# Performance work log

Hardware: AMD Instinct MI355X
Metric: run time of the kernel (lower is better)

Reference implementation:

```python
import jax, jax.numpy as jnp
import numpy as np

B, NO, NM, NV, E = 16, 512, 128, 64, 256
H, DK, MS, FF = 16, 16, 8, 512
TRANS_MAX = 100.0


def _ln(x):
    m = x.mean(-1, keepdims=True)
    v = ((x - m) ** 2).mean(-1, keepdims=True)
    return (x - m) * jax.lax.rsqrt(v + 1e-5)


def _inv_norm(x):
    # 1 - minmax-normalize over the whole per-batch matrix
    mn = x.min(axis=(1, 2), keepdims=True)
    mx = x.max(axis=(1, 2), keepdims=True)
    return 1.0 - (x - mn) / (mx - mn)


def _adjacency(proc_time, trans_time, MVpair_trans, mask_dyn, mask_ma):
    # masked copy of proc_time
    A_proc = jnp.where(mask_dyn, proc_time, 0.0)
    # keep only the per-row minimum nonzero entry (min_ProcTime_elements)
    nz = jnp.where(A_proc == 0.0, jnp.inf, A_proc)
    mn = nz.min(axis=2, keepdims=True)
    keep = (A_proc == mn) & (A_proc != 0.0)
    A_proc = A_proc * keep.astype(proc_time.dtype)
    A_proc_norm = (A_proc > 0.0).astype(proc_time.dtype)
    # machine-machine masks
    mask2 = mask_ma[:, None, :] & mask_ma[:, :, None]  # [B, nm, nm]
    A_procing = (~mask2).astype(proc_time.dtype)
    A_off = _inv_norm(MVpair_trans)
    tt = jnp.where(mask2, trans_time, TRANS_MAX + 1.0)
    A_on = _inv_norm(tt)
    return A_proc_norm, A_procing, A_off, A_on


def _block(row, col, cost, Wq, Wk, Wv, Wo, mW1, mb1, mW2, mb2, fW1, fb1, fW2, fb2):
    # MatNet-style mixed-score multi-head attention encoding block
    Bb, R, _ = row.shape
    C = col.shape[1]
    q = (row @ Wq).reshape(Bb, R, H, DK).transpose(0, 2, 1, 3)  # bhrd
    k = (col @ Wk).reshape(Bb, C, H, DK).transpose(0, 2, 1, 3)  # bhcd
    v = (col @ Wv).reshape(Bb, C, H, DK).transpose(0, 2, 1, 3)
    dot = jnp.einsum('bhrd,bhcd->bhrc', q, k) / jnp.sqrt(jnp.asarray(DK, row.dtype))
    two = jnp.stack([dot, jnp.broadcast_to(cost[:, None], dot.shape)], axis=-1)  # [B,H,R,C,2]
    hmix = jax.nn.relu(jnp.einsum('bhrct,hts->bhrcs', two, mW1) + mb1[None, :, None, None, :])
    score = jnp.einsum('bhrcs,hso->bhrco', hmix, mW2)[..., 0] + mb2[:, 0][None, :, None, None]
    attn = jax.nn.softmax(score, axis=-1)
    ctx = jnp.einsum('bhrc,bhcd->bhrd', attn, v).transpose(0, 2, 1, 3).reshape(Bb, R, H * DK)
    out1 = _ln(row + ctx @ Wo)
    ffn = jax.nn.relu(out1 @ fW1 + fb1) @ fW2 + fb2
    return _ln(out1 + ffn)


def setup_inputs() -> dict:
    key = jax.random.key(0)
    ks = jax.random.split(key, 24)

    def nrm(i, shape, s=0.05):
        return jax.random.normal(ks[i], shape, jnp.float32) * s

    return {
        'ope_emb': nrm(0, (B, NO, E), 1.0),
        'ma_emb': nrm(1, (B, NM, E), 1.0),
        'veh_emb': nrm(2, (B, NV, E), 1.0),
        'proc_time': jax.random.uniform(ks[3], (B, NO, NM), jnp.float32) * 20.0,
        'offload_trans_time': jax.random.uniform(ks[4], (B, NO, NV), jnp.float32) * TRANS_MAX,
        'trans_time': jax.random.uniform(ks[5], (B, NM, NM), jnp.float32) * TRANS_MAX,
        'MVpair_trans': jax.random.uniform(ks[6], (B, NV, NM), jnp.float32) * TRANS_MAX,
        'mask_dyn_ope_ma_adj': jax.random.bernoulli(ks[7], 0.3, (B, NO, NM)),
        'mask_ma': jax.random.bernoulli(ks[8], 0.7, (B, NM)),
        # stacked params for the 4 blocks: 0=ope, 1=veh, 2=ma1, 3=ma2
        'Wq': nrm(9, (4, E, H * DK)),
        'Wk': nrm(10, (4, E, H * DK)),
        'Wv': nrm(11, (4, E, H * DK)),
        'Wo': nrm(12, (4, H * DK, E)),
        'mixW1': nrm(13, (4, H, 2, MS), 0.3),
        'mixb1': jnp.zeros((4, H, MS), jnp.float32),
        'mixW2': nrm(14, (4, H, MS, 1), 0.3),
        'mixb2': jnp.zeros((4, H, 1), jnp.float32),
        'ffW1': nrm(15, (4, E, FF)),
        'ffb1': jnp.zeros((4, FF), jnp.float32),
        'ffW2': nrm(16, (4, FF, E)),
        'ffb2': jnp.zeros((4, E), jnp.float32),
        'maprojW': nrm(17, (2 * E, E)),
        'maprojb': jnp.zeros((E,), jnp.float32),
    }


def reference(ope_emb, ma_emb, veh_emb, proc_time, offload_trans_time, trans_time,
              MVpair_trans, mask_dyn_ope_ma_adj, mask_ma,
              Wq, Wk, Wv, Wo, mixW1, mixb1, mixW2, mixb2,
              ffW1, ffb1, ffW2, ffb2, maprojW, maprojb):
    A_proc_norm, A_procing, A_off, A_on = _adjacency(
        proc_time, trans_time, MVpair_trans, mask_dyn_ope_ma_adj, mask_ma)

    def blk(i, row, col, cost):
        return _block(row, col, cost, Wq[i], Wk[i], Wv[i], Wo[i],
                      mixW1[i], mixb1[i], mixW2[i], mixb2[i],
                      ffW1[i], ffb1[i], ffW2[i], ffb2[i])

    ope_out = blk(0, ope_emb, ma_emb, A_proc_norm)
    veh_out = blk(1, veh_emb, ma_emb, A_off)
    ma1 = blk(2, ma_emb, ma_emb, A_procing)
    ma2 = blk(3, ma_emb, ma_emb, A_on)
    ma_out = jnp.concatenate([ma1, ma2], axis=-1) @ maprojW + maprojb
    return (ope_out, ma_out, veh_out)
```

## Files before the change

kernel.cpp:

```cpp
#include <hip/hip_runtime.h>
#include <hip/hip_fp16.h>
#include <hip/hip_bf16.h>


typedef unsigned short u16;
typedef __attribute__((ext_vector_type(8))) short bf16x8;
typedef __attribute__((ext_vector_type(4))) float f32x4;
struct us4 { u16 x, y, z, w; };

__device__ __forceinline__ float bf2f(u16 u) {
  return __uint_as_float(((unsigned int)u) << 16);
}
__device__ __forceinline__ u16 f2bf(float f) {
  unsigned int x = __float_as_uint(f);
  x += 0x7FFFu + ((x >> 16) & 1u);
  return (u16)(x >> 16);
}
__device__ __forceinline__ __half2 h2max(__half2 a, __half2 b) {
  unsigned au = *(unsigned*)&a, bu = *(unsigned*)&b, ru;
  asm("v_pk_max_f16 %0, %1, %2" : "=v"(ru) : "v"(au), "v"(bu));
  return *(__half2*)&ru;
}

#define NBATCH 16
#define NOPE   512
#define NMA    128
#define NVEH   64
#define EDIM   256

struct PrepArgs {
  const float* ope; const float* ma; const float* veh;
  u16* ope_bf; u16* ma_bf; u16* veh_bf;
  const float* proc; const int* mask_dyn; float* A_proc;
  const float* mv; const float* trans; const int* mask_ma;
  unsigned int* mm;
};
struct TrArgs {
  const float* Wq; const float* Wk; const float* Wv; const float* Wo;
  const float* ffW1; const float* ffW2; const float* maproj;
  u16* WqT; u16* WkT; u16* WvT; u16* WoT; u16* ffW1T; u16* ffW2T; u16* maprojT;
};
__global__ __launch_bounds__(256) void prep_a(PrepArgs a, TrArgs tr) {
  int blk = blockIdx.x, t = threadIdx.x;
  if (blk < 2816) {
    int i = blk * 256 + t;
    const float* s; u16* d; int j;
    if (i < 524288)      { s = a.ope; d = a.ope_bf; j = i; }
    else if (i < 655360) { s = a.ma;  d = a.ma_bf;  j = i - 524288; }
    else                 { s = a.veh; d = a.veh_bf; j = i - 655360; }
    float4 v = ((const float4*)s)[j];
    us4 o = { f2bf(v.x), f2bf(v.y), f2bf(v.z), f2bf(v.w) };
    ((us4*)d)[j] = o;
    return;
  }
  if (blk < 6912) {
    int local = blk - 2816;
    int row = local * 2 + (t >> 7);
    int lane = t & 127;
    size_t idx = (size_t)row * NMA + lane;
    float av = a.mask_dyn[idx] ? a.proc[idx] : 0.0f;
    float cand = (av != 0.0f) ? av : 1.0e30f;
    __shared__ float red[256];
    red[t] = cand;
    __syncthreads();
    for (int s = 64; s > 0; s >>= 1) {
      if (lane < s) red[t] = fminf(red[t], red[t + s]);
      __syncthreads();
    }
    float mn = red[t & 128];
    a.A_proc[idx] = (av != 0.0f && av == mn) ? 1.0f : 0.0f;
    return;
  }
  if (blk < 7104) {
    __shared__ float smn[256], smx[256];
    float mn = 1.0e30f, mx = -1.0e30f;
    int mmIdx;
    if (blk < 6976) {
      int local = blk - 6912;
      int b = local >> 2, chunk = local & 3;
      const float* xb = a.mv + (size_t)b * 8192 + chunk * 2048;
#pragma unroll
      for (int r = 0; r < 8; r++) {
        float v = xb[r * 256 + t];
        mn = fminf(mn, v);
        mx = fmaxf(mx, v);
      }
      mmIdx = b;
    } else {
      int local = blk - 6976;
      int b = local >> 3, chunk = local & 7;
      __shared__ unsigned char mrow[NMA];
      if (t < NMA) mrow[t] = (unsigned char)(a.mask_ma[(size_t)b * NMA + t] != 0);
      __syncthreads();
      const float* tb = a.trans + (size_t)b * 16384 + chunk * 2048;
      int rbase = chunk * 16;
#pragma unroll
      for (int r = 0; r < 8; r++) {
        int off = r * 256 + t;
        int row = rbase + (off >> 7), col = off & 127;
        bool m2 = mrow[row] && mrow[col];
        float tt = m2 ? tb[off] : 101.0f;
        mn = fminf(mn, tt);
        mx = fmaxf(mx, tt);
      }
      mmIdx = 16 + b;
    }
    smn[t] = mn; smx[t] = mx;
    __syncthreads();
    for (int s = 128; s > 0; s >>= 1) {
      if (t < s) {
        smn[t] = fminf(smn[t], smn[t + s]);
        smx[t] = fmaxf(smx[t], smx[t + s]);
      }
      __syncthreads();
    }
    if (t == 0) {
      atomicMin(&a.mm[mmIdx], __float_as_uint(smn[0]));
      atomicMax(&a.mm[32 + mmIdx], __float_as_uint(smx[0]));
    }
    return;
  }
  {
    int b2 = blk - 7104;
    const float* src; u16* dst; int Kd, Nd, tile;
    if (b2 < 1024) {
      int w = b2 >> 8, i = (b2 >> 6) & 3; tile = b2 & 63;
      const float* sw = (w == 0 ? tr.Wq : w == 1 ? tr.Wk : w == 2 ? tr.Wv : tr.Wo);
      u16* dw = (w == 0 ? tr.WqT : w == 1 ? tr.WkT : w == 2 ? tr.WvT : tr.WoT);
      src = sw + (size_t)i * 65536; dst = dw + (size_t)i * 65536;
      Kd = 256; Nd = 256;
    } else if (b2 < 1536) {
      int z = (b2 - 1024) >> 7; tile = (b2 - 1024) & 127;
      src = tr.ffW1 + (size_t)z * 131072; dst = tr.ffW1T + (size_t)z * 131072;
      Kd = 256; Nd = 512;
    } else {
      int z = (b2 - 1536) >> 7; tile = (b2 - 1536) & 127;
      if (z < 4) { src = tr.ffW2 + (size_t)z * 131072; dst = tr.ffW2T + (size_t)z * 131072; }
      else       { src = tr.maproj; dst = tr.maprojT; }
      Kd = 512; Nd = 256;
    }
    int nx = Nd >> 5;
    int k0 = (tile / nx) * 32, n0 = (tile % nx) * 32;
    __shared__ float tl[32][33];
    int tx = t & 31, ty = t >> 5;
#pragma unroll
    for (int r = 0; r < 4; r++)
      tl[ty + r * 8][tx] = src[(size_t)(k0 + ty + r * 8) * Nd + n0 + tx];
    __syncthreads();
#pragma unroll
    for (int r = 0; r < 4; r++)
      dst[(size_t)(n0 + ty + r * 8) * Kd + k0 + tx] = f2bf(tl[tx][ty + r * 8]);
  }
}

struct PB {
  const float* mv; const float* trans; const int* mask_ma;
  const unsigned int* mm; float* A_offb; float* a_on; float* a_pcing;
};
__device__ __forceinline__ void prep_b_body(const PB& p, int blk, int t) {
  if (blk < 512) {
    int b = blk >> 5, off = (blk & 31) * 256 + t;
    float lo = __uint_as_float(p.mm[b]);
    float inv = 1.0f / (__uint_as_float(p.mm[32 + b]) - lo);
    size_t idx = (size_t)b * 8192 + off;
    p.A_offb[idx] = 1.0f - (p.mv[idx] - lo) * inv;
    return;
  }
  int local = blk - 512;
  int b = local >> 6, off = (local & 63) * 256 + t;
  int row = off >> 7, col = off & 127;
  bool m2 = (p.mask_ma[(size_t)b * NMA + row] != 0) &&
            (p.mask_ma[(size_t)b * NMA + col] != 0);
  size_t idx = (size_t)b * 16384 + off;
  float tt = m2 ? p.trans[idx] : 101.0f;
  float lo = __uint_as_float(p.mm[16 + b]);
  float inv = 1.0f / (__uint_as_float(p.mm[48 + b]) - lo);
  p.a_on[idx] = 1.0f - (tt - lo) * inv;
  p.a_pcing[idx] = m2 ? 0.0f : 1.0f;
}

struct GG {
  const u16* A; const u16* WT; const float* bias; u16* C;
  int M, N, K, epi, wgStart, cshift, mode;
};
struct GGArgs { GG g[12]; PB pb; int n; int nGemmWG; };

__global__ __launch_bounds__(256) void gemm_grouped(GGArgs args) {
  int wg = blockIdx.x;
  if (wg >= args.nGemmWG) {
    prep_b_body(args.pb, wg - args.nGemmWG, threadIdx.x);
    return;
  }
  int gi = 0;
  for (int i = 1; i < args.n; i++)
    if (wg >= args.g[i].wgStart) gi = i;
  GG gg = args.g[gi];
  int lwg = wg - gg.wgStart;
  int bx = lwg & ((1 << gg.cshift) - 1);
  int by = lwg >> gg.cshift;
  int N = gg.N, K = gg.K;

  __shared__ u16 As[128][40];
  __shared__ u16 Bs[128][40];
  int tid = threadIdx.x;
  int lane = tid & 63, wid = tid >> 6;
  int wr = (wid >> 1) * 64, wc = (wid & 1) * 64;
  int m16 = lane & 15, quad = lane >> 4;
  int rb = by * 128, cb = bx * 128;
  int srow = tid >> 2;
  int schunk = (tid & 3) * 8;

  f32x4 acc[4][4];
#pragma unroll
  for (int i = 0; i < 4; i++)
#pragma unroll
    for (int j = 0; j < 4; j++) acc[i][j] = (f32x4){0.f, 0.f, 0.f, 0.f};

  for (int k0 = 0; k0 < K; k0 += 32) {
    uint4 va0 = *(const uint4*)(gg.A + (size_t)(rb + srow) * K + k0 + schunk);
    uint4 va1 = *(const uint4*)(gg.A + (size_t)(rb + 64 + srow) * K + k0 + schunk);
    uint4 vb0 = *(const uint4*)(gg.WT + (size_t)(cb + srow) * K + k0 + schunk);
    uint4 vb1 = *(const uint4*)(gg.WT + (size_t)(cb + 64 + srow) * K + k0 + schunk);
    __syncthreads();
    *(uint4*)&As[srow][schunk] = va0;
    *(uint4*)&As[64 + srow][schunk] = va1;
    *(uint4*)&Bs[srow][schunk] = vb0;
    *(uint4*)&Bs[64 + srow][schunk] = vb1;
    __syncthreads();
    bf16x8 af[4], bfr[4];
#pragma unroll
    for (int i = 0; i < 4; i++)
      af[i] = *(const bf16x8*)&As[wr + i * 16 + m16][quad * 8];
#pragma unroll
    for (int j = 0; j < 4; j++)
      bfr[j] = *(const bf16x8*)&Bs[wc + j * 16 + m16][quad * 8];
#pragma unroll
    for (int i = 0; i < 4; i++)
#pragma unroll
      for (int j = 0; j < 4; j++)
        acc[i][j] = __builtin_amdgcn_mfma_f32_16x16x32_bf16(
            af[i], bfr[j], acc[i][j], 0, 0, 0);
  }

#pragma unroll
  for (int i = 0; i < 4; i++) {
#pragma unroll
    for (int j = 0; j < 4; j++) {
      int col = cb + wc + j * 16 + m16;
      float bv = (gg.epi >= 1) ? gg.bias[col] : 0.0f;
      if (gg.mode == 3) {
        int row0 = rb + wr + i * 16 + quad * 4;
        int b = row0 >> 7, c0 = row0 & 127;
        us4 o = { f2bf(acc[i][j][0]), f2bf(acc[i][j][1]),
                  f2bf(acc[i][j][2]), f2bf(acc[i][j][3]) };
        *(us4*)(gg.C + (size_t)b * 32768 + (size_t)col * 128 + c0) = o;
      } else {
#pragma unroll
        for (int r = 0; r < 4; r++) {
          int row = rb + wr + i * 16 + quad * 4 + r;
          float v = acc[i][j][r] + bv;
          if (gg.epi == 2) v = fmaxf(v, 0.0f);
          size_t off;
          if (gg.mode == 0) {
            off = (size_t)row * N + col;
          } else if (gg.mode == 1) {
            off = ((size_t)(row >> 4)) * 4096 + (size_t)(col >> 4) * 256 +
                  (size_t)(row & 15) * 16 + (col & 15);
          } else {
            off = ((size_t)(row >> 7)) * 32768 + (size_t)(col >> 4) * 2048 +
                  (size_t)(row & 127) * 16 + (col & 15);
          }
          gg.C[off] = f2bf(v);
        }
      }
    }
  }
}

__global__ __launch_bounds__(256) void gemm_mfma_f32(
    const u16* __restrict__ A, const u16* __restrict__ WT,
    const float* __restrict__ bias, float* __restrict__ C,
    int M, int N, int K) {
  __shared__ u16 As[64][40];
  __shared__ u16 Bs[64][40];
  int tid = threadIdx.x;
  int lane = tid & 63, wid = tid >> 6;
  int wr = (wid >> 1) * 32, wc = (wid & 1) * 32;
  int m16 = lane & 15, quad = lane >> 4;
  int rb = blockIdx.y * 64, cb = blockIdx.x * 64;
  int srow = tid >> 2;
  int schunk = (tid & 3) * 8;
  f32x4 acc[2][2];
#pragma unroll
  for (int i = 0; i < 2; i++)
#pragma unroll
    for (int j = 0; j < 2; j++) acc[i][j] = (f32x4){0.f, 0.f, 0.f, 0.f};
  for (int k0 = 0; k0 < K; k0 += 32) {
    uint4 va = *(const uint4*)(A + (size_t)(rb + srow) * K + k0 + schunk);
    uint4 vb = *(const uint4*)(WT + (size_t)(cb + srow) * K + k0 + schunk);
    __syncthreads();
    *(uint4*)&As[srow][schunk] = va;
    *(uint4*)&Bs[srow][schunk] = vb;
    __syncthreads();
    bf16x8 af[2], bfr[2];
#pragma unroll
    for (int i = 0; i < 2; i++)
      af[i] = *(const bf16x8*)&As[wr + i * 16 + m16][quad * 8];
#pragma unroll
    for (int j = 0; j < 2; j++)
      bfr[j] = *(const bf16x8*)&Bs[wc + j * 16 + m16][quad * 8];
#pragma unroll
    for (int i = 0; i < 2; i++)
#pragma unroll
      for (int j = 0; j < 2; j++)
        acc[i][j] = __builtin_amdgcn_mfma_f32_16x16x32_bf16(
            af[i], bfr[j], acc[i][j], 0, 0, 0);
  }
#pragma unroll
  for (int i = 0; i < 2; i++)
#pragma unroll
    for (int j = 0; j < 2; j++) {
      int col = cb + wc + j * 16 + m16;
      float bv = bias[col];
#pragma unroll
      for (int r = 0; r < 4; r++) {
        int row = rb + wr + i * 16 + quad * 4 + r;
        C[(size_t)row * N + col] = acc[i][j][r] + bv;
      }
    }
}

struct AG {
  const u16* q; const u16* k; const u16* vT; const float* cost; u16* ctx;
  const float* w1; const float* b1; const float* w2; const float* b2;
  int R, wgStart;
};
struct AGArgs { AG g[4]; };

#define CSTRIDE 134

__global__ __launch_bounds__(256) void attn_grouped(AGArgs args) {
  int blk = blockIdx.x;
  int gi = 0;
#pragma unroll
  for (int i = 1; i < 4; i++)
    if (blk >= args.g[i].wgStart) gi = i;
  AG gg = args.g[gi];
  int local = blk - gg.wgStart;

  int t = threadIdx.x;
  int wave = t >> 6, lane = t & 63;
  int quad = lane >> 4, l16 = lane & 15;
  int j = local & 15;
  int b = (j & 7) * 2 + (j >> 3);
  int hgrp = (local >> 4) & 1;
  int tile = local >> 5;
  int m0 = b * gg.R + tile * 16;

  __shared__ __half costs_h[16 * CSTRIDE];
  __shared__ u16 pbuf[4][16 * 136];

  const float* cp = gg.cost + (size_t)m0 * 128;
  for (int i = t; i < 2048; i += 256)
    costs_h[(i >> 7) * CSTRIDE + (i & 127)] = __float2half(cp[i]);
  __syncthreads();

  const bf16x8 zerof = (bf16x8){0, 0, 0, 0, 0, 0, 0, 0};
  const f32x4 zacc = (f32x4){0.f, 0.f, 0.f, 0.f};
  const __half2 zh = __float2half2_rn(0.0f);
  u16* pb = pbuf[wave];
  const u16* qtile = gg.q + ((size_t)(m0 >> 4)) * 4096;
  const u16* kb    = gg.k + (size_t)b * 32768;

#pragma unroll
  for (int hh = 0; hh < 2; hh++) {
    int h = hgrp * 8 + wave * 2 + hh;

    __half2 w10h[8], w11h[8], b1h[8], w2h[8];
#pragma unroll
    for (int s = 0; s < 8; s++) {
      w10h[s] = __float2half2_rn(gg.w1[h * 16 + s] * 0.25f);
      w11h[s] = __float2half2_rn(gg.w1[h * 16 + 8 + s]);
      b1h[s]  = __float2half2_rn(gg.b1[h * 8 + s]);
      w2h[s]  = __float2half2_rn(gg.w2[h * 8 + s]);
    }
    float wb2v = gg.b2[h];

    bf16x8 bq = zerof;
    if (quad < 2)
      bq = *(const bf16x8*)(qtile + (size_t)h * 256 + l16 * 16 + quad * 8);
    f32x4 st[8];
    __builtin_amdgcn_s_setprio(1);
#pragma unroll
    for (int ct = 0; ct < 8; ct++) {
      bf16x8 ak = zerof;
      if (quad < 2)
        ak = *(const bf16x8*)(kb + (size_t)h * 2048 + (ct * 16 + l16) * 16 +
                              quad * 8);
      st[ct] = __builtin_amdgcn_mfma_f32_16x16x32_bf16(ak, bq, zacc, 0, 0, 0);
    }
    __builtin_amdgcn_s_setprio(0);

#pragma unroll
    for (int ct = 0; ct < 8; ct++) {
#pragma unroll
      for (int p = 0; p < 2; p++) {
        __half2 d2 = __float22half2_rn(
            make_float2(st[ct][p * 2], st[ct][p * 2 + 1]));
        __half2 c2 = *(const __half2*)&costs_h[l16 * CSTRIDE + ct * 16 +
                                               quad * 4 + p * 2];
        __half2 s2 = zh;
#pragma unroll
        for (int s = 0; s < 8; s++) {
          __half2 hm = __hfma2(d2, w10h[s], __hfma2(c2, w11h[s], b1h[s]));
          hm = h2max(hm, zh);
          s2 = __hfma2(hm, w2h[s], s2);
        }
        float2 sf = __half22float2(s2);
        st[ct][p * 2]     = sf.x + wb2v;
        st[ct][p * 2 + 1] = sf.y + wb2v;
      }
    }

    float mx = -1.0e30f;
#pragma unroll
    for (int ct = 0; ct < 8; ct++)
#pragma unroll
      for (int rg = 0; rg < 4; rg++) mx = fmaxf(mx, st[ct][rg]);
    mx = fmaxf(mx, __shfl_xor(mx, 16, 64));
    mx = fmaxf(mx, __shfl_xor(mx, 32, 64));
    float sum = 0.0f;
#pragma unroll
    for (int ct = 0; ct < 8; ct++)
#pragma unroll
      for (int rg = 0; rg < 4; rg++) {
        float e = __expf(st[ct][rg] - mx);
        st[ct][rg] = e;
        sum += e;
      }
    sum += __shfl_xor(sum, 16, 64);
    sum += __shfl_xor(sum, 32, 64);
    float inv = 1.0f / sum;

#pragma unroll
    for (int ct = 0; ct < 8; ct++) {
#pragma unroll
      for (int p = 0; p < 2; p++) {
        __hip_bfloat162 pk = __float22bfloat162_rn(
            make_float2(st[ct][p * 2] * inv, st[ct][p * 2 + 1] * inv));
        *(unsigned int*)&pb[l16 * 136 + ct * 16 + quad * 4 + p * 2] =
            *(unsigned int*)&pk;
      }
    }

    f32x4 cacc = zacc;
    __builtin_amdgcn_s_setprio(1);
#pragma unroll
    for (int ks = 0; ks < 4; ks++) {
      bf16x8 ap = *(const bf16x8*)&pb[l16 * 136 + ks * 32 + quad * 8];
      bf16x8 bv = *(const bf16x8*)(gg.vT + (size_t)b * 32768 +
                                   (size_t)(h * 16 + l16) * 128 + ks * 32 +
                                   quad * 8);
      cacc = __builtin_amdgcn_mfma_f32_16x16x32_bf16(ap, bv, cacc, 0, 0, 0);
    }
    __builtin_amdgcn_s_setprio(0);

#pragma unroll
    for (int rg = 0; rg < 4; rg++)
      gg.ctx[(size_t)(m0 + quad * 4 + rg) * 256 + h * 16 + l16] =
          f2bf(cacc[rg]);
  }
}

struct LN1Args {
  const float* r0; const float* r1; const float* r2; const float* r3;
  int s1, s2, s3;
};
__global__ __launch_bounds__(256) void ln1_grouped(
    LN1Args a, const u16* __restrict__ x, u16* __restrict__ out) {
  int row = blockIdx.x * 4 + (threadIdx.x >> 6);
  int lane = threadIdx.x & 63;
  const float* resid;
  int local;
  if (row < a.s1)      { resid = a.r0; local = row; }
  else if (row < a.s2) { resid = a.r1; local = row - a.s1; }
  else if (row < a.s3) { resid = a.r2; local = row - a.s2; }
  else                 { resid = a.r3; local = row - a.s3; }
  float4 rv = *(const float4*)(resid + (size_t)local * 256 + lane * 4);
  us4 xv = *(const us4*)(x + (size_t)row * 256 + lane * 4);
  float v0 = rv.x + bf2f(xv.x);
  float v1 = rv.y + bf2f(xv.y);
  float v2 = rv.z + bf2f(xv.z);
  float v3 = rv.w + bf2f(xv.w);
  float s  = v0 + v1 + v2 + v3;
  float ss = v0 * v0 + v1 * v1 + v2 * v2 + v3 * v3;
#pragma unroll
  for (int d = 1; d < 64; d <<= 1) {
    s  += __shfl_xor(s, d, 64);
    ss += __shfl_xor(ss, d, 64);
  }
  float mean = s * (1.0f / 256.0f);
  float var = ss * (1.0f / 256.0f) - mean * mean;
  float rs = rsqrtf(fmaxf(var, 0.0f) + 1e-5f);
  us4 o = { f2bf((v0 - mean) * rs), f2bf((v1 - mean) * rs),
            f2bf((v2 - mean) * rs), f2bf((v3 - mean) * rs) };
  *(us4*)(out + (size_t)row * 256 + lane * 4) = o;
}

struct LN2Args {
  float* f0; float* f1; u16* b2; u16* b3;
  int s1, s2, s3;
};
__global__ __launch_bounds__(256) void ln2_grouped(
    LN2Args a, const u16* __restrict__ resid, const u16* __restrict__ x) {
  int row = blockIdx.x * 4 + (threadIdx.x >> 6);
  int lane = threadIdx.x & 63;
  us4 rv = *(const us4*)(resid + (size_t)row * 256 + lane * 4);
  us4 xv = *(const us4*)(x + (size_t)row * 256 + lane * 4);
  float v0 = bf2f(rv.x) + bf2f(xv.x);
  float v1 = bf2f(rv.y) + bf2f(xv.y);
  float v2 = bf2f(rv.z) + bf2f(xv.z);
  float v3 = bf2f(rv.w) + bf2f(xv.w);
  float s  = v0 + v1 + v2 + v3;
  float ss = v0 * v0 + v1 * v1 + v2 * v2 + v3 * v3;
#pragma unroll
  for (int d = 1; d < 64; d <<= 1) {
    s  += __shfl_xor(s, d, 64);
    ss += __shfl_xor(ss, d, 64);
  }
  float mean = s * (1.0f / 256.0f);
  float var = ss * (1.0f / 256.0f) - mean * mean;
  float rs = rsqrtf(fmaxf(var, 0.0f) + 1e-5f);
  float y0 = (v0 - mean) * rs, y1 = (v1 - mean) * rs;
  float y2 = (v2 - mean) * rs, y3 = (v3 - mean) * rs;
  if (row < a.s1) {
    float4 o = {y0, y1, y2, y3};
    *(float4*)(a.f0 + (size_t)row * 256 + lane * 4) = o;
  } else if (row < a.s2) {
    float4 o = {y0, y1, y2, y3};
    *(float4*)(a.f1 + (size_t)(row - a.s1) * 256 + lane * 4) = o;
  } else if (row < a.s3) {
    us4 o = { f2bf(y0), f2bf(y1), f2bf(y2), f2bf(y3) };
    *(us4*)(a.b2 + (size_t)(row - a.s2) * 512 + lane * 4) = o;
  } else {
    us4 o = { f2bf(y0), f2bf(y1), f2bf(y2), f2bf(y3) };
    *(us4*)(a.b3 + (size_t)(row - a.s3) * 512 + 256 + lane * 4) = o;
  }
}

extern "C" void kernel_launch(void* const* d_in, const int* in_sizes, int n_in,
                              void* d_out, int out_size, void* d_ws, size_t ws_size,
                              hipStream_t stream) {
  const float* ope   = (const float*)d_in[0];
  const float* ma    = (const float*)d_in[1];
  const float* veh   = (const float*)d_in[2];
  const float* proc  = (const float*)d_in[3];
  const float* trans = (const float*)d_in[5];
  const float* mv    = (const float*)d_in[6];
  const int* mask_dyn = (const int*)d_in[7];
  const int* mask_ma  = (const int*)d_in[8];
  const float* Wq = (const float*)d_in[9];
  const float* Wk = (const float*)d_in[10];
  const float* Wv = (const float*)d_in[11];
  const float* Wo = (const float*)d_in[12];
  const float* mixW1 = (const float*)d_in[13];
  const float* mixb1 = (const float*)d_in[14];
  const float* mixW2 = (const float*)d_in[15];
  const float* mixb2 = (const float*)d_in[16];
  const float* ffW1 = (const float*)d_in[17];
  const float* ffb1 = (const float*)d_in[18];
  const float* ffW2 = (const float*)d_in[19];
  const float* ffb2 = (const float*)d_in[20];
  const float* maprojW = (const float*)d_in[21];
  const float* maprojb = (const float*)d_in[22];
  float* out = (float*)d_out;
  char* ws = (char*)d_ws;

  const int OFF[4] = {0, 8192, 9216, 11264};
  const int MS4[4] = {8192, 1024, 2048, 2048};
  const int TOT = 13312;

  const size_t MB = 1 << 20;
  float* A_proc  = (float*)(ws + 0);
  float* A_offb  = (float*)(ws + 4 * MB);
  float* A_pcing = (float*)(ws + 4 * MB + MB / 2);
  float* A_on    = (float*)(ws + 5 * MB + MB / 2);
  u16* ope_bf  = (u16*)(ws + 6 * MB + MB / 2);
  u16* ma_bf   = (u16*)(ws + 10 * MB + MB / 2);
  u16* veh_bf  = (u16*)(ws + 11 * MB + MB / 2);
  u16* WqT     = (u16*)(ws + 12 * MB);
  u16* WkT     = (u16*)(ws + 12 * MB + MB / 2);
  u16* WvT     = (u16*)(ws + 13 * MB);
  u16* WoT     = (u16*)(ws + 13 * MB + MB / 2);
  u16* ffW1T   = (u16*)(ws + 14 * MB);
  u16* ffW2T   = (u16*)(ws + 15 * MB);
  u16* maprojT = (u16*)(ws + 16 * MB);
  u16* q_all   = (u16*)(ws + 16 * MB + MB / 2);
  u16* k_all   = (u16*)(ws + 23 * MB);
  u16* vT_all  = (u16*)(ws + 31 * MB);
  u16* ctx_all = (u16*)(ws + 35 * MB);
  u16* t1_all  = (u16*)(ws + 41 * MB + MB / 2);
  u16* out1_all= (u16*)(ws + 48 * MB);
  u16* ffh_all = (u16*)(ws + 54 * MB + MB / 2);
  u16* maCat   = (u16*)(ws + 67 * MB + MB / 2);
  unsigned int* mmbuf = (unsigned int*)(ws + 70 * MB);

  hipMemsetAsync(mmbuf, 0x7F, 128, stream);
  hipMemsetAsync((char*)mmbuf + 128, 0x00, 128, stream);

  {
    PrepArgs pa = {ope, ma, veh, ope_bf, ma_bf, veh_bf,
                   proc, mask_dyn, A_proc, mv, trans, mask_ma, mmbuf};
    TrArgs ta = {Wq, Wk, Wv, Wo, ffW1, ffW2, maprojW,
                 WqT, WkT, WvT, WoT, ffW1T, ffW2T, maprojT};
    prep_a<<<9280, 256, 0, stream>>>(pa, ta);
  }

  const size_t MA_OUT  = (size_t)NBATCH * NOPE * EDIM;
  const size_t VEH_OUT = MA_OUT + (size_t)NBATCH * NMA * EDIM;

  const u16* rowbf[4] = {ope_bf, veh_bf, ma_bf, ma_bf};
  const float* costp[4] = {A_proc, A_offb, A_pcing, A_on};
  PB pb = {mv, trans, mask_ma, mmbuf, A_offb, A_on, A_pcing};

  {
    GGArgs ga; ga.n = 12; ga.pb = pb;
    int wg = 0;
    for (int i = 0; i < 4; i++) {
      ga.g[i] = {rowbf[i], WqT + (size_t)i * 65536, nullptr,
                 q_all + (size_t)OFF[i] * 256, MS4[i], 256, 256, 0, wg, 1, 1};
      wg += (MS4[i] / 128) * 2;
    }
    for (int i = 0; i < 4; i++) {
      ga.g[4 + i] = {ma_bf, WkT + (size_t)i * 65536, nullptr,
                     k_all + (size_t)i * 524288, 2048, 256, 256, 0, wg, 1, 2};
      wg += 32;
    }
    for (int i = 0; i < 4; i++) {
      ga.g[8 + i] = {ma_bf, WvT + (size_t)i * 65536, nullptr,
                     vT_all + (size_t)i * 524288, 2048, 256, 256, 0, wg, 1, 3};
      wg += 32;
    }
    ga.nGemmWG = wg;
    gemm_grouped<<<wg + 1536, 256, 0, stream>>>(ga);
  }

  {
    AGArgs aa;
    int wg = 0;
    const int R4[4] = {NOPE, NVEH, NMA, NMA};
    for (int i = 0; i < 4; i++) {
      aa.g[i] = {q_all + (size_t)OFF[i] * 256, k_all + (size_t)i * 524288,
                 vT_all + (size_t)i * 524288, costp[i],
                 ctx_all + (size_t)OFF[i] * 256,
                 mixW1 + (size_t)i * 256, mixb1 + (size_t)i * 128,
                 mixW2 + (size_t)i * 128, mixb2 + (size_t)i * 16,
                 R4[i], wg};
      wg += MS4[i] / 8;
    }
    attn_grouped<<<wg, 256, 0, stream>>>(aa);
  }

  {
    GGArgs ga; ga.n = 4; ga.pb = pb;
    int wg = 0;
    for (int i = 0; i < 4; i++) {
      ga.g[i] = {ctx_all + (size_t)OFF[i] * 256, WoT + (size_t)i * 65536,
                 nullptr, t1_all + (size_t)OFF[i] * 256,
                 MS4[i], 256, 256, 0, wg, 1, 0};
      wg += (MS4[i] / 128) * 2;
    }
    ga.nGemmWG = wg;
    gemm_grouped<<<wg, 256, 0, stream>>>(ga);
  }

  {
    LN1Args la = {ope, veh, ma, ma, 8192, 9216, 11264};
    ln1_grouped<<<TOT / 4, 256, 0, stream>>>(la, t1_all, out1_all);
  }

  {
    GGArgs ga; ga.n = 4; ga.pb = pb;
    int wg = 0;
    for (int i = 0; i < 4; i++) {
      ga.g[i] = {out1_all + (size_t)OFF[i] * 256, ffW1T + (size_t)i * 131072,
                 ffb1 + (size_t)i * 512, ffh_all + (size_t)OFF[i] * 512,
                 MS4[i], 512, 256, 2, wg, 2, 0};
      wg += (MS4[i] / 128) * 4;
    }
    ga.nGemmWG = wg;
    gemm_grouped<<<wg, 256, 0, stream>>>(ga);
  }

  {
    GGArgs ga; ga.n = 4; ga.pb = pb;
    int wg = 0;
    for (int i = 0; i < 4; i++) {
      ga.g[i] = {ffh_all + (size_t)OFF[i] * 512, ffW2T + (size_t)i * 131072,
                 ffb2 + (size_t)i * 256, t1_all + (size_t)OFF[i] * 256,
                 MS4[i], 256, 512, 1, wg, 1, 0};
      wg += (MS4[i] / 128) * 2;
    }
    ga.nGemmWG = wg;
    gemm_grouped<<<wg, 256, 0, stream>>>(ga);
  }

  {
    LN2Args la = {out, out + VEH_OUT, maCat, maCat, 8192, 9216, 11264};
    ln2_grouped<<<TOT / 4, 256, 0, stream>>>(la, out1_all, t1_all);
  }

  gemm_mfma_f32<<<dim3(4, 32), 256, 0, stream>>>(maCat, maprojT, maprojb,
      out + MA_OUT, 2048, 256, 512);
}
```

Measured before the change: 252.9 us.

## Fuse Wo projection, layernorms and FFN into a single per-row-tile kernel

Replaces the output-projection GEMM, first layernorm, two FFN GEMMs and second layernorm with one kernel that processes 64-row tiles end to end, keeping the intermediate activations in shared memory. This removes four kernel launches and the global-memory round trips of the t1/out1/ffh intermediates. In exchange the grid shrinks to 208 workgroups, each doing all three GEMMs serially with a short K step and frequent barriers, which may leave compute units underused.

```diff
diff --git a/kernel.cpp b/kernel.cpp
--- a/kernel.cpp
+++ b/kernel.cpp
@@ -472,80 +472,256 @@
   }
 }
 
-struct LN1Args {
-  const float* r0; const float* r1; const float* r2; const float* r3;
-  int s1, s2, s3;
+struct FTArgs {
+  const u16* ctx;
+  const float* rope; const float* rveh; const float* rma;
+  const u16* WoT; const u16* W1T; const u16* W2T;
+  const float* ffb1; const float* ffb2;
+  float* outOpe; float* outVeh; u16* maCat;
 };
-__global__ __launch_bounds__(256) void ln1_grouped(
-    LN1Args a, const u16* __restrict__ x, u16* __restrict__ out) {
-  int row = blockIdx.x * 4 + (threadIdx.x >> 6);
-  int lane = threadIdx.x & 63;
-  const float* resid;
-  int local;
-  if (row < a.s1)      { resid = a.r0; local = row; }
-  else if (row < a.s2) { resid = a.r1; local = row - a.s1; }
-  else if (row < a.s3) { resid = a.r2; local = row - a.s2; }
-  else                 { resid = a.r3; local = row - a.s3; }
-  float4 rv = *(const float4*)(resid + (size_t)local * 256 + lane * 4);
-  us4 xv = *(const us4*)(x + (size_t)row * 256 + lane * 4);
-  float v0 = rv.x + bf2f(xv.x);
-  float v1 = rv.y + bf2f(xv.y);
-  float v2 = rv.z + bf2f(xv.z);
-  float v3 = rv.w + bf2f(xv.w);
-  float s  = v0 + v1 + v2 + v3;
-  float ss = v0 * v0 + v1 * v1 + v2 * v2 + v3 * v3;
-#pragma unroll
-  for (int d = 1; d < 64; d <<= 1) {
-    s  += __shfl_xor(s, d, 64);
-    ss += __shfl_xor(ss, d, 64);
-  }
-  float mean = s * (1.0f / 256.0f);
-  float var = ss * (1.0f / 256.0f) - mean * mean;
-  float rs = rsqrtf(fmaxf(var, 0.0f) + 1e-5f);
-  us4 o = { f2bf((v0 - mean) * rs), f2bf((v1 - mean) * rs),
-            f2bf((v2 - mean) * rs), f2bf((v3 - mean) * rs) };
-  *(us4*)(out + (size_t)row * 256 + lane * 4) = o;
-}
-
-struct LN2Args {
-  float* f0; float* f1; u16* b2; u16* b3;
-  int s1, s2, s3;
-};
-__global__ __launch_bounds__(256) void ln2_grouped(
-    LN2Args a, const u16* __restrict__ resid, const u16* __restrict__ x) {
-  int row = blockIdx.x * 4 + (threadIdx.x >> 6);
-  int lane = threadIdx.x & 63;
-  us4 rv = *(const us4*)(resid + (size_t)row * 256 + lane * 4);
-  us4 xv = *(const us4*)(x + (size_t)row * 256 + lane * 4);
-  float v0 = bf2f(rv.x) + bf2f(xv.x);
-  float v1 = bf2f(rv.y) + bf2f(xv.y);
-  float v2 = bf2f(rv.z) + bf2f(xv.z);
-  float v3 = bf2f(rv.w) + bf2f(xv.w);
-  float s  = v0 + v1 + v2 + v3;
-  float ss = v0 * v0 + v1 * v1 + v2 * v2 + v3 * v3;
-#pragma unroll
-  for (int d = 1; d < 64; d <<= 1) {
-    s  += __shfl_xor(s, d, 64);
-    ss += __shfl_xor(ss, d, 64);
-  }
-  float mean = s * (1.0f / 256.0f);
-  float var = ss * (1.0f / 256.0f) - mean * mean;
-  float rs = rsqrtf(fmaxf(var, 0.0f) + 1e-5f);
-  float y0 = (v0 - mean) * rs, y1 = (v1 - mean) * rs;
-  float y2 = (v2 - mean) * rs, y3 = (v3 - mean) * rs;
-  if (row < a.s1) {
-    float4 o = {y0, y1, y2, y3};
-    *(float4*)(a.f0 + (size_t)row * 256 + lane * 4) = o;
-  } else if (row < a.s2) {
-    float4 o = {y0, y1, y2, y3};
-    *(float4*)(a.f1 + (size_t)(row - a.s1) * 256 + lane * 4) = o;
-  } else if (row < a.s3) {
-    us4 o = { f2bf(y0), f2bf(y1), f2bf(y2), f2bf(y3) };
-    *(us4*)(a.b2 + (size_t)(row - a.s2) * 512 + lane * 4) = o;
-  } else {
-    us4 o = { f2bf(y0), f2bf(y1), f2bf(y2), f2bf(y3) };
-    *(us4*)(a.b3 + (size_t)(row - a.s3) * 512 + 256 + lane * 4) = o;
-  }
+
+__global__ __launch_bounds__(256) void fused_tail(FTArgs a) {
+  int rb = blockIdx.x * 64;
+  int gi = (rb < 8192) ? 0 : (rb < 9216) ? 1 : (rb < 11264) ? 2 : 3;
+  const u16* WoT = a.WoT + (size_t)gi * 65536;
+  const u16* W1T = a.W1T + (size_t)gi * 131072;
+  const u16* W2T = a.W2T + (size_t)gi * 131072;
+  const float* b1p = a.ffb1 + gi * 512;
+  const float* b2p = a.ffb2 + gi * 256;
+  const float* resid; int lr0;
+  if (gi == 0)      { resid = a.rope; lr0 = rb; }
+  else if (gi == 1) { resid = a.rveh; lr0 = rb - 8192; }
+  else if (gi == 2) { resid = a.rma;  lr0 = rb - 9216; }
+  else              { resid = a.rma;  lr0 = rb - 11264; }
+
+  __shared__ u16 O1[64][264];
+  __shared__ u16 Fs[64][520];
+  __shared__ u16 Asg[64][40];
+  __shared__ u16 Bsg[256][40];
+  __shared__ float redS[64][4];
+  __shared__ float redQ[64][4];
+
+  int tid = threadIdx.x;
+  int lane = tid & 63, wid = tid >> 6;
+  int m16 = lane & 15, quad = lane >> 4;
+  int wc = wid * 64;
+  int srow = tid >> 2, schunk = (tid & 3) * 8;
+
+  f32x4 acc[4][4];
+#pragma unroll
+  for (int i = 0; i < 4; i++)
+#pragma unroll
+    for (int j = 0; j < 4; j++) acc[i][j] = (f32x4){0.f, 0.f, 0.f, 0.f};
+
+  uint4 va = *(const uint4*)(a.ctx + (size_t)(rb + srow) * 256 + schunk);
+  uint4 vb[4];
+#pragma unroll
+  for (int c = 0; c < 4; c++)
+    vb[c] = *(const uint4*)(WoT + (size_t)(c * 64 + srow) * 256 + schunk);
+  for (int k0 = 0; k0 < 256; k0 += 32) {
+    __syncthreads();
+    *(uint4*)&Asg[srow][schunk] = va;
+#pragma unroll
+    for (int c = 0; c < 4; c++)
+      *(uint4*)&Bsg[c * 64 + srow][schunk] = vb[c];
+    if (k0 + 32 < 256) {
+      va = *(const uint4*)(a.ctx + (size_t)(rb + srow) * 256 + k0 + 32 + schunk);
+#pragma unroll
+      for (int c = 0; c < 4; c++)
+        vb[c] = *(const uint4*)(WoT + (size_t)(c * 64 + srow) * 256 + k0 + 32 + schunk);
+    }
+    __syncthreads();
+    bf16x8 af[4], bf[4];
+#pragma unroll
+    for (int i = 0; i < 4; i++)
+      af[i] = *(const bf16x8*)&Asg[i * 16 + m16][quad * 8];
+#pragma unroll
+    for (int j = 0; j < 4; j++)
+      bf[j] = *(const bf16x8*)&Bsg[wc + j * 16 + m16][quad * 8];
+#pragma unroll
+    for (int i = 0; i < 4; i++)
+#pragma unroll
+      for (int j = 0; j < 4; j++)
+        acc[i][j] = __builtin_amdgcn_mfma_f32_16x16x32_bf16(
+            af[i], bf[j], acc[i][j], 0, 0, 0);
+  }
+
+#pragma unroll
+  for (int i = 0; i < 4; i++)
+#pragma unroll
+    for (int j = 0; j < 4; j++) {
+      int colj = wc + j * 16 + m16;
+#pragma unroll
+      for (int r = 0; r < 4; r++)
+        acc[i][j][r] += resid[(size_t)(lr0 + i * 16 + quad * 4 + r) * 256 + colj];
+    }
+#pragma unroll
+  for (int i = 0; i < 4; i++)
+#pragma unroll
+    for (int r = 0; r < 4; r++) {
+      float s = acc[i][0][r] + acc[i][1][r] + acc[i][2][r] + acc[i][3][r];
+      float q = acc[i][0][r] * acc[i][0][r] + acc[i][1][r] * acc[i][1][r] +
+                acc[i][2][r] * acc[i][2][r] + acc[i][3][r] * acc[i][3][r];
+#pragma unroll
+      for (int d = 1; d < 16; d <<= 1) {
+        s += __shfl_xor(s, d, 64);
+        q += __shfl_xor(q, d, 64);
+      }
+      if (m16 == 0) {
+        redS[i * 16 + quad * 4 + r][wid] = s;
+        redQ[i * 16 + quad * 4 + r][wid] = q;
+      }
+    }
+  __syncthreads();
+#pragma unroll
+  for (int i = 0; i < 4; i++)
+#pragma unroll
+    for (int r = 0; r < 4; r++) {
+      int row = i * 16 + quad * 4 + r;
+      float s = redS[row][0] + redS[row][1] + redS[row][2] + redS[row][3];
+      float q = redQ[row][0] + redQ[row][1] + redQ[row][2] + redQ[row][3];
+      float mean = s * (1.0f / 256.0f);
+      float var = q * (1.0f / 256.0f) - mean * mean;
+      float rs = rsqrtf(fmaxf(var, 0.0f) + 1e-5f);
+#pragma unroll
+      for (int j = 0; j < 4; j++)
+        O1[row][wc + j * 16 + m16] = f2bf((acc[i][j][r] - mean) * rs);
+    }
+
+  for (int p = 0; p < 2; p++) {
+#pragma unroll
+    for (int i = 0; i < 4; i++)
+#pragma unroll
+      for (int j = 0; j < 4; j++) acc[i][j] = (f32x4){0.f, 0.f, 0.f, 0.f};
+#pragma unroll
+    for (int c = 0; c < 4; c++)
+      vb[c] = *(const uint4*)(W1T + (size_t)(p * 256 + c * 64 + srow) * 256 + schunk);
+    for (int k0 = 0; k0 < 256; k0 += 32) {
+      __syncthreads();
+#pragma unroll
+      for (int c = 0; c < 4; c++)
+        *(uint4*)&Bsg[c * 64 + srow][schunk] = vb[c];
+      if (k0 + 32 < 256) {
+#pragma unroll
+        for (int c = 0; c < 4; c++)
+          vb[c] = *(const uint4*)(W1T + (size_t)(p * 256 + c * 64 + srow) * 256 +
+                                  k0 + 32 + schunk);
+      }
+      __syncthreads();
+      bf16x8 af[4], bf[4];
+#pragma unroll
+      for (int i = 0; i < 4; i++)
+        af[i] = *(const bf16x8*)&O1[i * 16 + m16][k0 + quad * 8];
+#pragma unroll
+      for (int j = 0; j < 4; j++)
+        bf[j] = *(const bf16x8*)&Bsg[wc + j * 16 + m16][quad * 8];
+#pragma unroll
+      for (int i = 0; i < 4; i++)
+#pragma unroll
+        for (int j = 0; j < 4; j++)
+          acc[i][j] = __builtin_amdgcn_mfma_f32_16x16x32_bf16(
+              af[i], bf[j], acc[i][j], 0, 0, 0);
+    }
+#pragma unroll
+    for (int i = 0; i < 4; i++)
+#pragma unroll
+      for (int j = 0; j < 4; j++) {
+        int col = p * 256 + wc + j * 16 + m16;
+        float bv = b1p[col];
+#pragma unroll
+        for (int r = 0; r < 4; r++)
+          Fs[i * 16 + quad * 4 + r][col] = f2bf(fmaxf(acc[i][j][r] + bv, 0.0f));
+      }
+  }
+
+#pragma unroll
+  for (int i = 0; i < 4; i++)
+#pragma unroll
+    for (int j = 0; j < 4; j++) acc[i][j] = (f32x4){0.f, 0.f, 0.f, 0.f};
+#pragma unroll
+  for (int c = 0; c < 4; c++)
+    vb[c] = *(const uint4*)(W2T + (size_t)(c * 64 + srow) * 512 + schunk);
+  for (int k0 = 0; k0 < 512; k0 += 32) {
+    __syncthreads();
+#pragma unroll
+    for (int c = 0; c < 4; c++)
+      *(uint4*)&Bsg[c * 64 + srow][schunk] = vb[c];
+    if (k0 + 32 < 512) {
+#pragma unroll
+      for (int c = 0; c < 4; c++)
+        vb[c] = *(const uint4*)(W2T + (size_t)(c * 64 + srow) * 512 +
+                                k0 + 32 + schunk);
+    }
+    __syncthreads();
+    bf16x8 af[4], bf[4];
+#pragma unroll
+    for (int i = 0; i < 4; i++)
+      af[i] = *(const bf16x8*)&Fs[i * 16 + m16][k0 + quad * 8];
+#pragma unroll
+    for (int j = 0; j < 4; j++)
+      bf[j] = *(const bf16x8*)&Bsg[wc + j * 16 + m16][quad * 8];
+#pragma unroll
+    for (int i = 0; i < 4; i++)
+#pragma unroll
+      for (int j = 0; j < 4; j++)
+        acc[i][j] = __builtin_amdgcn_mfma_f32_16x16x32_bf16(
+            af[i], bf[j], acc[i][j], 0, 0, 0);
+  }
+
+#pragma unroll
+  for (int i = 0; i < 4; i++)
+#pragma unroll
+    for (int j = 0; j < 4; j++) {
+      int colj = wc + j * 16 + m16;
+      float bv = b2p[colj];
+#pragma unroll
+      for (int r = 0; r < 4; r++) {
+        int row = i * 16 + quad * 4 + r;
+        acc[i][j][r] += bv + bf2f(O1[row][colj]);
+      }
+    }
+#pragma unroll
+  for (int i = 0; i < 4; i++)
+#pragma unroll
+    for (int r = 0; r < 4; r++) {
+      float s = acc[i][0][r] + acc[i][1][r] + acc[i][2][r] + acc[i][3][r];
+      float q = acc[i][0][r] * acc[i][0][r] + acc[i][1][r] * acc[i][1][r] +
+                acc[i][2][r] * acc[i][2][r] + acc[i][3][r] * acc[i][3][r];
+#pragma unroll
+      for (int d = 1; d < 16; d <<= 1) {
+        s += __shfl_xor(s, d, 64);
+        q += __shfl_xor(q, d, 64);
+      }
+      if (m16 == 0) {
+        redS[i * 16 + quad * 4 + r][wid] = s;
+        redQ[i * 16 + quad * 4 + r][wid] = q;
+      }
+    }
+  __syncthreads();
+#pragma unroll
+  for (int i = 0; i < 4; i++)
+#pragma unroll
+    for (int r = 0; r < 4; r++) {
+      int row = i * 16 + quad * 4 + r;
+      float s = redS[row][0] + redS[row][1] + redS[row][2] + redS[row][3];
+      float q = redQ[row][0] + redQ[row][1] + redQ[row][2] + redQ[row][3];
+      float mean = s * (1.0f / 256.0f);
+      float var = q * (1.0f / 256.0f) - mean * mean;
+      float rs = rsqrtf(fmaxf(var, 0.0f) + 1e-5f);
+#pragma unroll
+      for (int j = 0; j < 4; j++) {
+        int colj = wc + j * 16 + m16;
+        float y = (acc[i][j][r] - mean) * rs;
+        if (gi == 0)
+          a.outOpe[(size_t)(lr0 + row) * 256 + colj] = y;
+        else if (gi == 1)
+          a.outVeh[(size_t)(lr0 + row) * 256 + colj] = y;
+        else if (gi == 2)
+          a.maCat[(size_t)(lr0 + row) * 512 + colj] = f2bf(y);
+        else
+          a.maCat[(size_t)(lr0 + row) * 512 + 256 + colj] = f2bf(y);
+      }
+    }
 }
 
 extern "C" void kernel_launch(void* const* d_in, const int* in_sizes, int n_in,
@@ -578,7 +754,6 @@
 
   const int OFF[4] = {0, 8192, 9216, 11264};
   const int MS4[4] = {8192, 1024, 2048, 2048};
-  const int TOT = 13312;
 
   const size_t MB = 1 << 20;
   float* A_proc  = (float*)(ws + 0);
@@ -599,9 +774,6 @@
   u16* k_all   = (u16*)(ws + 23 * MB);
   u16* vT_all  = (u16*)(ws + 31 * MB);
   u16* ctx_all = (u16*)(ws + 35 * MB);
-  u16* t1_all  = (u16*)(ws + 41 * MB + MB / 2);
-  u16* out1_all= (u16*)(ws + 48 * MB);
-  u16* ffh_all = (u16*)(ws + 54 * MB + MB / 2);
   u16* maCat   = (u16*)(ws + 67 * MB + MB / 2);
   unsigned int* mmbuf = (unsigned int*)(ws + 70 * MB);
 
@@ -662,52 +834,9 @@
   }
 
   {
-    GGArgs ga; ga.n = 4; ga.pb = pb;
-    int wg = 0;
-    for (int i = 0; i < 4; i++) {
-      ga.g[i] = {ctx_all + (size_t)OFF[i] * 256, WoT + (size_t)i * 65536,
-                 nullptr, t1_all + (size_t)OFF[i] * 256,
-                 MS4[i], 256, 256, 0, wg, 1, 0};
-      wg += (MS4[i] / 128) * 2;
-    }
-    ga.nGemmWG = wg;
-    gemm_grouped<<<wg, 256, 0, stream>>>(ga);
-  }
-
-  {
-    LN1Args la = {ope, veh, ma, ma, 8192, 9216, 11264};
-    ln1_grouped<<<TOT / 4, 256, 0, stream>>>(la, t1_all, out1_all);
-  }
-
-  {
-    GGArgs ga; ga.n = 4; ga.pb = pb;
-    int wg = 0;
-    for (int i = 0; i < 4; i++) {
-      ga.g[i] = {out1_all + (size_t)OFF[i] * 256, ffW1T + (size_t)i * 131072,
-                 ffb1 + (size_t)i * 512, ffh_all + (size_t)OFF[i] * 512,
-                 MS4[i], 512, 256, 2, wg, 2, 0};
-      wg += (MS4[i] / 128) * 4;
-    }
-    ga.nGemmWG = wg;
-    gemm_grouped<<<wg, 256, 0, stream>>>(ga);
-  }
-
-  {
-    GGArgs ga; ga.n = 4; ga.pb = pb;
-    int wg = 0;
-    for (int i = 0; i < 4; i++) {
-      ga.g[i] = {ffh_all + (size_t)OFF[i] * 512, ffW2T + (size_t)i * 131072,
-                 ffb2 + (size_t)i * 256, t1_all + (size_t)OFF[i] * 256,
-                 MS4[i], 256, 512, 1, wg, 1, 0};
-      wg += (MS4[i] / 128) * 2;
-    }
-    ga.nGemmWG = wg;
-    gemm_grouped<<<wg, 256, 0, stream>>>(ga);
-  }
-
-  {
-    LN2Args la = {out, out + VEH_OUT, maCat, maCat, 8192, 9216, 11264};
-    ln2_grouped<<<TOT / 4, 256, 0, stream>>>(la, out1_all, t1_all);
+    FTArgs fa = {ctx_all, ope, veh, ma, WoT, ffW1T, ffW2T, ffb1, ffb2,
+                 out, out + VEH_OUT, maCat};
+    fused_tail<<<208, 256, 0, stream>>>(fa);
   }
 
   gemm_mfma_f32<<<dim3(4, 32), 256, 0, stream>>>(maCat, maprojT, maprojb,
```

Result: faster. 246.4 us (-2.6%).
